# Performance work log

Measured on AMD Instinct MI355X. Metric: run time of the kernel, lower is better.

## Reference

```python
import jax, jax.numpy as jnp
import numpy as np

B, N, C, K = 16, 2048, 64, 20
RED = 16  # SE reduction


def setup_inputs() -> dict:
    key = jax.random.key(0)
    ks = jax.random.split(key, 8)
    x = jax.random.normal(ks[0], (B * N, C), dtype=jnp.float32)
    batch = jnp.repeat(jnp.arange(B, dtype=jnp.int64), N)
    s1 = 1.0 / np.sqrt(2 * C)
    s2 = 1.0 / np.sqrt(C)
    W1 = jax.random.normal(ks[1], (2 * C, C), dtype=jnp.float32) * s1
    b1 = jnp.zeros((C,), dtype=jnp.float32)
    W2 = jax.random.normal(ks[2], (C, C), dtype=jnp.float32) * s2
    b2 = jnp.zeros((C,), dtype=jnp.float32)
    W3 = jax.random.normal(ks[3], (C, C), dtype=jnp.float32) * s2
    b3 = jnp.zeros((C,), dtype=jnp.float32)
    se_w1 = jax.random.normal(ks[4], (C, C // RED), dtype=jnp.float32) * s2
    se_w2 = jax.random.normal(ks[5], (C // RED, C), dtype=jnp.float32) * (1.0 / np.sqrt(C // RED))
    sa_w = jax.random.normal(ks[6], (1, 2, 7), dtype=jnp.float32) * (1.0 / np.sqrt(14))
    return {"x": x, "batch": batch, "batch_size": B, "W1": W1, "b1": b1,
            "W2": W2, "b2": b2, "W3": W3, "b3": b3,
            "se_w1": se_w1, "se_w2": se_w2, "sa_w": sa_w}


def _forward(x, batch_size, W1, b1, W2, b2, W3, b3, se_w1, se_w2, sa_w):
    n = x.shape[0] // batch_size
    xb = x.reshape(batch_size, n, -1)              # [B,N,C]
    # --- dynamic kNN graph (self point included, as in PyG knn) ---
    sq = jnp.sum(xb * xb, axis=-1)                 # [B,N]
    d = sq[:, :, None] + sq[:, None, :] - 2.0 * jnp.einsum('bic,bjc->bij', xb, xb)
    _, idx = jax.lax.top_k(-d, K)                  # [B,N,K] nearest (incl self)
    xj = jax.vmap(lambda pts, ids: pts[ids])(xb, idx)   # [B,N,K,C]
    xi = xb[:, :, None, :]
    edge = jnp.concatenate([jnp.broadcast_to(xi, xj.shape), xj - xi], axis=-1)  # [B,N,K,2C]
    # --- shared edge MLP ---
    h = jax.nn.relu(edge @ W1 + b1)
    h = jax.nn.relu(h @ W2 + b2)
    h = h @ W3 + b3                                 # [B,N,K,C]
    agg = jnp.max(h, axis=2)                        # [B,N,C] max-aggregate
    # --- SE channel attention (pool over points) ---
    s = jnp.mean(agg, axis=1)                       # [B,C]
    y = jax.nn.sigmoid(jax.nn.relu(s @ se_w1) @ se_w2)  # [B,C]
    x_se = agg * y[:, None, :]
    # --- spatial attention (pool over channels, conv1d k=7) ---
    avg_out = jnp.mean(x_se, axis=2)                # [B,N]
    max_out = jnp.max(x_se, axis=2)                 # [B,N]
    ycat = jnp.stack([avg_out, max_out], axis=1)    # [B,2,N]
    att = jax.lax.conv_general_dilated(ycat, sa_w, (1,), [(3, 3)],
                                       dimension_numbers=('NCH', 'OIH', 'NCH'))  # [B,1,N]
    att = jax.nn.sigmoid(att)
    x_att = x_se * att.transpose(0, 2, 1)           # [B,N,C]
    # --- residual (in_channels == out_channels) ---
    out = x_att + xb
    return out.reshape(batch_size * n, -1)


def reference(x, batch, batch_size, W1, b1, W2, b2, W3, b3, se_w1, se_w2, sa_w):
    return _forward(x, batch_size, W1, b1, W2, b2, W3, b3, se_w1, se_w2, sa_w)
```

## Files before the change

### kernel.cpp

```cpp
#include <hip/hip_runtime.h>

typedef unsigned int uint32;
typedef unsigned long long uint64;
typedef unsigned short ushortT;
typedef __attribute__((ext_vector_type(8))) short short8;
typedef __attribute__((ext_vector_type(4))) short short4v;
typedef __attribute__((ext_vector_type(4))) float floatx4;

#define DEV static __device__ __forceinline__

#define NN 2048
#define CC 64
#define KK 20

DEV float bf2f(ushortT h) {
  union { uint32 u; float f; } c; c.u = ((uint32)h) << 16; return c.f;
}
DEV ushortT f2bf(float f) {
  union { float f; uint32 u; } c; c.f = f;
  uint32 r = c.u + 0x7FFFu + ((c.u >> 16) & 1u);
  return (ushortT)(r >> 16);
}
DEV void split2(float v, ushortT& h, ushortT& l) {
  h = f2bf(v);
  l = f2bf(v - bf2f(h));
}
DEV uint32 fmap(float f) {
  uint32 u = __float_as_uint(f);
  return (u & 0x80000000u) ? ~u : (u | 0x80000000u);
}
DEV float funmap(uint32 m) {
  uint32 u = (m & 0x80000000u) ? (m ^ 0x80000000u) : ~m;
  return __uint_as_float(u);
}
DEV short8 ld8(const ushortT* p) {
  short4v a = *(const short4v*)p;
  short4v b = *(const short4v*)(p + 4);
  short8 r;
  r[0] = a.x; r[1] = a.y; r[2] = a.z; r[3] = a.w;
  r[4] = b.x; r[5] = b.y; r[6] = b.z; r[7] = b.w;
  return r;
}

__global__ void k_sq(const float* __restrict__ x, float* __restrict__ sq,
                     ushortT* __restrict__ xbf) {
  int p = blockIdx.x * 256 + threadIdx.x;
  const float4* row = (const float4*)(x + (size_t)p * CC);
  ushortT* orow = xbf + (size_t)p * CC;
  float s = 0.f;
#pragma unroll
  for (int q = 0; q < 16; ++q) {
    float4 v = row[q];
    s += v.x * v.x + v.y * v.y + v.z * v.z + v.w * v.w;
    short4v h;
    h.x = (short)f2bf(v.x); h.y = (short)f2bf(v.y);
    h.z = (short)f2bf(v.z); h.w = (short)f2bf(v.w);
    *(short4v*)(orow + q * 4) = h;
  }
  sq[p] = s;
}

__global__ void k_wconv(const float* __restrict__ w1, const float* __restrict__ w2,
                        const float* __restrict__ w3, ushortT* __restrict__ wbf) {
  int t = threadIdx.x;
  for (int e = t; e < 4096; e += 256) {
    int n = e >> 6, k = e & 63;
    wbf[e]         = f2bf(w1[k * 64 + n]);
    wbf[4096 + e]  = f2bf(w1[(64 + k) * 64 + n]);
    wbf[8192 + e]  = f2bf(w2[k * 64 + n]);
    wbf[12288 + e] = f2bf(w3[k * 64 + n]);
  }
}

__launch_bounds__(256, 4)
__global__ void k_knn(const ushortT* __restrict__ xbf, const float* __restrict__ sq,
                      ushortT* __restrict__ cand) {
  const int b  = blockIdx.y;
  const int i0 = blockIdx.x * 32;
  const int t  = threadIdx.x;
  const int l  = t & 63, wv = t >> 6;
  const int la = l & 15, quad = l >> 4;
  const int pp = t >> 2, ss = t & 3;

  __shared__ __align__(16) char sm[35968];
  ushortT (*sXj)[72]    = (ushortT(*)[72])(sm);
  uint32  (*sCand)[130] = (uint32(*)[130])(sm + 18432);
  uint32*  sTau         = (uint32*)(sm + 35072);
  uint32*  sCnt         = (uint32*)(sm + 35200);
  float*   sSqi         = (float*)(sm + 35328);
  float*   sSqj         = (float*)(sm + 35456);

  const ushortT* xbb = xbf + ((size_t)b * NN) * CC;

  const int mw  = wv & 1;
  const int nt0 = (wv >> 1) * 4;

  short8 afrag[2];
  {
    const ushortT* rowp = xbb + (size_t)(i0 + mw * 16 + la) * CC;
#pragma unroll
    for (int ks = 0; ks < 2; ++ks)
      afrag[ks] = *(const short8*)(rowp + ks * 32 + quad * 8);
  }
  if (t < 32) sSqi[t] = sq[b * NN + i0 + t];

  {
    int r = t >> 1, co = (t & 1) * 32;
    const ushortT* src = xbb + (size_t)r * CC + co;
#pragma unroll
    for (int i = 0; i < 4; ++i)
      *(uint4*)&sXj[r][co + i * 8] = *(const uint4*)(src + i * 8);
  }
  if (t < 128) sSqj[t] = sq[b * NN + t];

  uint32 lst[KK];
#pragma unroll
  for (int s = 0; s < KK; ++s) lst[s] = 0xFFFFFFFFu;

  __syncthreads();

  float sqa[4];
  {
    float4 v = *(const float4*)&sSqi[mw * 16 + quad * 4];
    sqa[0] = v.x; sqa[1] = v.y; sqa[2] = v.z; sqa[3] = v.w;
  }

  for (int jt = 0; jt < 16; ++jt) {
    const int j0 = jt * 128;

    floatx4 acc[4];
#pragma unroll
    for (int n = 0; n < 4; ++n) acc[n] = (floatx4){0.f, 0.f, 0.f, 0.f};

#pragma unroll
    for (int ks = 0; ks < 2; ++ks) {
      int kof = ks * 32 + quad * 8;
#pragma unroll
      for (int n = 0; n < 4; ++n) {
        short8 bv = *(const short8*)&sXj[(nt0 + n) * 16 + la][kof];
        acc[n] = __builtin_amdgcn_mfma_f32_16x16x32_bf16(afrag[ks], bv, acc[n], 0, 0, 0);
      }
    }

    if (jt == 0) {
#pragma unroll
      for (int n = 0; n < 4; ++n) {
        int jl = (nt0 + n) * 16 + la;
        float dj = sSqj[jl];
        uint32 jg = (uint32)(j0 + jl);
#pragma unroll
        for (int rg = 0; rg < 4; ++rg) {
          int il = mw * 16 + quad * 4 + rg;
          float d = fmaxf(sqa[rg] + dj - 2.0f * acc[n][rg], 0.f);
          sCand[il][jl] = (__float_as_uint(d) & 0xFFFFF800u) | jg;
        }
      }
    } else {
      uint32 tv[4];
      {
        uint4 u = *(const uint4*)&sTau[mw * 16 + quad * 4];
        tv[0] = u.x; tv[1] = u.y; tv[2] = u.z; tv[3] = u.w;
      }
#pragma unroll
      for (int n = 0; n < 4; ++n) {
        int jl = (nt0 + n) * 16 + la;
        float dj = sSqj[jl];
        uint32 jg = (uint32)(j0 + jl);
#pragma unroll
        for (int rg = 0; rg < 4; ++rg) {
          int il = mw * 16 + quad * 4 + rg;
          float d = fmaxf(sqa[rg] + dj - 2.0f * acc[n][rg], 0.f);
          uint32 key = (__float_as_uint(d) & 0xFFFFF800u) | jg;
          if (key < tv[rg]) {
            uint32 slot = atomicAdd(&sCnt[il], 1u);
            sCand[il][slot] = key;
          }
        }
      }
    }
    __syncthreads();

    if (t < 128) {
      int cnt = (jt == 0) ? 128 : (int)sCnt[pp];
      for (int q = ss; q < cnt; q += 4) {
        uint32 cur = sCand[pp][q];
#pragma unroll
        for (int s = 0; s < KK; ++s) {
          uint32 lo = min(lst[s], cur);
          cur = max(lst[s], cur);
          lst[s] = lo;
        }
      }
      uint32 m19 = lst[KK - 1];
      m19 = min(m19, (uint32)__shfl_xor((int)m19, 1));
      m19 = min(m19, (uint32)__shfl_xor((int)m19, 2));
      if (ss == 0) { sTau[pp] = m19; sCnt[pp] = 0u; }
    }

    if (jt < 15) {
      const int jn = (jt + 1) * 128;
      int r = t >> 1, co = (t & 1) * 32;
      const ushortT* src = xbb + (size_t)(jn + r) * CC + co;
#pragma unroll
      for (int i = 0; i < 4; ++i)
        *(uint4*)&sXj[r][co + i * 8] = *(const uint4*)(src + i * 8);
      if (t < 128) sSqj[t] = sq[b * NN + jn + t];
    }
    __syncthreads();
  }

  if (t < 128) {
    size_t base = ((size_t)(b * NN + i0 + pp)) * 80 + ss * KK;
#pragma unroll
    for (int s = 0; s < KK; ++s) cand[base + s] = (ushortT)(lst[s] & 2047u);
  }
}

__launch_bounds__(256, 4)
__global__ void k_rerank(const float* __restrict__ x, const ushortT* __restrict__ cand,
                         int* __restrict__ idxout) {
  const int b  = blockIdx.y;
  const int i0 = blockIdx.x * 16;
  const int t  = threadIdx.x;
  const int grp = t >> 4, lg = t & 15;

  __shared__ double sK[16][81];

  const float* xb = x + ((size_t)b * NN) * CC;
  const int p = i0 + grp;
  float4 vi = ((const float4*)(xb + (size_t)p * CC))[lg];
  size_t cb = ((size_t)(b * NN + p)) * 80;

  const bool hi8 = (lg & 8) != 0;
  const bool hi4 = (lg & 4) != 0;
  const bool hi2 = (lg & 2) != 0;
  const int  uslot = ((lg >> 1) & 1) | (((lg >> 2) & 1) << 1) | (((lg >> 3) & 1) << 2);

  for (int q0 = 0; q0 < 80; q0 += 8) {
    int jj0 = (int)cand[cb + q0 + 0], jj1 = (int)cand[cb + q0 + 1];
    int jj2 = (int)cand[cb + q0 + 2], jj3 = (int)cand[cb + q0 + 3];
    int jj4 = (int)cand[cb + q0 + 4], jj5 = (int)cand[cb + q0 + 5];
    int jj6 = (int)cand[cb + q0 + 6], jj7 = (int)cand[cb + q0 + 7];

#define DISTQ(JJ, DD)                                                        \
    double DD;                                                               \
    {                                                                        \
      float4 vj = ((const float4*)(xb + (size_t)(JJ) * CC))[lg];             \
      double e0 = (double)vi.x - (double)vj.x;                               \
      double e1 = (double)vi.y - (double)vj.y;                               \
      double e2 = (double)vi.z - (double)vj.z;                               \
      double e3 = (double)vi.w - (double)vj.w;                               \
      DD = e0 * e0 + e1 * e1 + e2 * e2 + e3 * e3;                            \
    }
    DISTQ(jj0, dd0) DISTQ(jj1, dd1) DISTQ(jj2, dd2) DISTQ(jj3, dd3)
    DISTQ(jj4, dd4) DISTQ(jj5, dd5) DISTQ(jj6, dd6) DISTQ(jj7, dd7)
#undef DISTQ

    double m0 = hi8 ? dd4 : dd0, s0 = hi8 ? dd0 : dd4;
    double m1 = hi8 ? dd5 : dd1, s1 = hi8 ? dd1 : dd5;
    double m2 = hi8 ? dd6 : dd2, s2 = hi8 ? dd2 : dd6;
    double m3 = hi8 ? dd7 : dd3, s3 = hi8 ? dd3 : dd7;
    double r40 = m0 + __shfl_xor(s0, 8, 16);
    double r41 = m1 + __shfl_xor(s1, 8, 16);
    double r42 = m2 + __shfl_xor(s2, 8, 16);
    double r43 = m3 + __shfl_xor(s3, 8, 16);
    int j40 = hi8 ? jj4 : jj0, j41 = hi8 ? jj5 : jj1;
    int j42 = hi8 ? jj6 : jj2, j43 = hi8 ? jj7 : jj3;

    double n0 = hi4 ? r42 : r40, t0 = hi4 ? r40 : r42;
    double n1 = hi4 ? r43 : r41, t1 = hi4 ? r41 : r43;
    double r20 = n0 + __shfl_xor(t0, 4, 16);
    double r21 = n1 + __shfl_xor(t1, 4, 16);
    int j20 = hi4 ? j42 : j40, j21 = hi4 ? j43 : j41;

    double p0 = hi2 ? r21 : r20, u0 = hi2 ? r20 : r21;
    double r1 = p0 + __shfl_xor(u0, 2, 16);
    int j1 = hi2 ? j21 : j20;

    r1 += __shfl_xor(r1, 1, 16);

    if ((lg & 1) == 0) {
      uint64 bits = (uint64)__double_as_longlong(r1);
      sK[grp][q0 + uslot] = __longlong_as_double((bits & ~2047ULL) | (uint64)j1);
    }
  }
  __syncthreads();

  double k5[5];
#pragma unroll
  for (int s = 0; s < 5; ++s) k5[s] = sK[grp][lg + 16 * s];

  const double DINF = __longlong_as_double(0x7FF0000000000000LL);
  size_t obase = ((size_t)(b * NN + p)) * KK;
  for (int r = 0; r < KK; ++r) {
    double lm = fmin(fmin(fmin(k5[0], k5[1]), fmin(k5[2], k5[3])), k5[4]);
#pragma unroll
    for (int off = 8; off > 0; off >>= 1)
      lm = fmin(lm, __shfl_xor(lm, off, 16));
#pragma unroll
    for (int s = 0; s < 5; ++s) k5[s] = (k5[s] == lm) ? DINF : k5[s];
    if (lg == (r & 15))
      idxout[obase + r] = (int)((uint64)__double_as_longlong(lm) & 2047ULL);
  }
}

__launch_bounds__(256, 4)
__global__ void k_mlp(const float* __restrict__ x, const ushortT* __restrict__ xbf,
                      const int* __restrict__ idx, const ushortT* __restrict__ wbf,
                      const float* __restrict__ b1, const float* __restrict__ b2,
                      const float* __restrict__ b3, float* __restrict__ agg) {
  const int b  = blockIdx.y;
  const int i0 = blockIdx.x * 4;
  const int t  = threadIdx.x;
  const int l  = t & 63, wv = t >> 6;
  const int la = l & 15, quad = l >> 4;

  __shared__ __align__(16) char sm[35008];
  ushortT (*sDH)[68]  = (ushortT(*)[68])(sm + 0);
  ushortT (*sDL)[68]  = (ushortT(*)[68])(sm + 10880);
  ushortT (*sH1)[68]  = (ushortT(*)[68])(sm + 21760);
  float   (*sPre)[64] = (float(*)[64])(sm + 32640);
  uint32*  sAgg       = (uint32*)(sm + 33664);
  int*     sJ         = (int*)(sm + 34688);
  ushortT (*sH2)[68]  = sDH;

  const int c = wv * 16 + la;
  const ushortT* w1aT = wbf;
  const ushortT* w1bT = wbf + 4096;
  const ushortT* w2T  = wbf + 8192;
  const ushortT* w3T  = wbf + 12288;

  if (t < 80) {
    int p = t / 20, kk = t - p * 20;
    int v = idx[((size_t)(b * NN + i0 + p)) * KK + kk];
    v = v < 0 ? 0 : (v > (NN - 1) ? (NN - 1) : v);
    sJ[t] = v;
  }
  sAgg[t] = 0u;

  float b2c = b2[c], b3c = b3[c];

  {
    float b1c = b1[c];
    floatx4 ap = (floatx4){b1c, b1c, b1c, b1c};
#pragma unroll
    for (int ks = 0; ks < 2; ++ks) {
      short8 av = *(const short8*)(xbf + (size_t)(b * NN + i0 + (la & 3)) * CC + ks * 32 + quad * 8);
      short8 bv = *(const short8*)(w1aT + c * 64 + ks * 32 + quad * 8);
      ap = __builtin_amdgcn_mfma_f32_16x16x32_bf16(av, bv, ap, 0, 0, 0);
    }
    if (quad == 0) {
#pragma unroll
      for (int rg = 0; rg < 4; ++rg) sPre[rg][c] = ap[rg];
    }
  }
  __syncthreads();

  const float* xb = x + ((size_t)b * NN) * CC;
  for (int e = t; e < 1280; e += 256) {
    int r = e >> 4, c4g = e & 15, c4 = c4g * 4;
    int p = r / 20;
    float4 vi = ((const float4*)(xb + (size_t)(i0 + p) * CC))[c4g];
    float4 vj = ((const float4*)(xb + (size_t)sJ[r] * CC))[c4g];
    short4v dh, dl;
    ushortT hh, ll;
    split2(vj.x - vi.x, hh, ll); dh.x = (short)hh; dl.x = (short)ll;
    split2(vj.y - vi.y, hh, ll); dh.y = (short)hh; dl.y = (short)ll;
    split2(vj.z - vi.z, hh, ll); dh.z = (short)hh; dl.z = (short)ll;
    split2(vj.w - vi.w, hh, ll); dh.w = (short)hh; dl.w = (short)ll;
    *(short4v*)&sDH[r][c4] = dh;
    *(short4v*)&sDL[r][c4] = dl;
  }
  __syncthreads();

  {
    short8 bB[2];
#pragma unroll
    for (int ks = 0; ks < 2; ++ks)
      bB[ks] = *(const short8*)(w1bT + c * 64 + ks * 32 + quad * 8);
#pragma unroll
    for (int m5 = 0; m5 < 5; ++m5) {
      floatx4 a;
#pragma unroll
      for (int rg = 0; rg < 4; ++rg) {
        int r = m5 * 16 + quad * 4 + rg;
        a[rg] = sPre[r / 20][c];
      }
#pragma unroll
      for (int ks = 0; ks < 2; ++ks) {
        int kof = ks * 32 + quad * 8;
        short8 aDH = ld8(&sDH[m5 * 16 + la][kof]);
        short8 aDL = ld8(&sDL[m5 * 16 + la][kof]);
        a = __builtin_amdgcn_mfma_f32_16x16x32_bf16(aDH, bB[ks], a, 0, 0, 0);
        a = __builtin_amdgcn_mfma_f32_16x16x32_bf16(aDL, bB[ks], a, 0, 0, 0);
      }
#pragma unroll
      for (int rg = 0; rg < 4; ++rg) {
        int r = m5 * 16 + quad * 4 + rg;
        sH1[r][c] = f2bf(fmaxf(a[rg], 0.f));
      }
    }
  }
  __syncthreads();

  {
    short8 bf[2];
#pragma unroll
    for (int ks = 0; ks < 2; ++ks)
      bf[ks] = *(const short8*)(w2T + c * 64 + ks * 32 + quad * 8);
#pragma unroll
    for (int m5 = 0; m5 < 5; ++m5) {
      floatx4 a = (floatx4){b2c, b2c, b2c, b2c};
#pragma unroll
      for (int ks = 0; ks < 2; ++ks) {
        short8 aH = ld8(&sH1[m5 * 16 + la][ks * 32 + quad * 8]);
        a = __builtin_amdgcn_mfma_f32_16x16x32_bf16(aH, bf[ks], a, 0, 0, 0);
      }
#pragma unroll
      for (int rg = 0; rg < 4; ++rg) {
        int r = m5 * 16 + quad * 4 + rg;
        sH2[r][c] = f2bf(fmaxf(a[rg], 0.f));
      }
    }
  }
  __syncthreads();

  {
    short8 bf[2];
#pragma unroll
    for (int ks = 0; ks < 2; ++ks)
      bf[ks] = *(const short8*)(w3T + c * 64 + ks * 32 + quad * 8);
#pragma unroll
    for (int m5 = 0; m5 < 5; ++m5) {
      floatx4 a = (floatx4){b3c, b3c, b3c, b3c};
#pragma unroll
      for (int ks = 0; ks < 2; ++ks) {
        short8 aH = ld8(&sH2[m5 * 16 + la][ks * 32 + quad * 8]);
        a = __builtin_amdgcn_mfma_f32_16x16x32_bf16(aH, bf[ks], a, 0, 0, 0);
      }
#pragma unroll
      for (int rg = 0; rg < 4; ++rg) {
        int r = m5 * 16 + quad * 4 + rg;
        int p = r / 20;
        atomicMax(&sAgg[p * 64 + c], fmap(a[rg]));
      }
    }
  }
  __syncthreads();

  {
    int p = t >> 6, cc = t & 63;
    agg[((size_t)(b * NN + i0 + p)) * CC + cc] = funmap(sAgg[t]);
  }
}

__global__ void k_se1(const float* __restrict__ agg, float* __restrict__ part) {
  int b = blockIdx.x >> 4, ch = blockIdx.x & 15;
  int t = threadIdx.x;
  int c = t & 63, q = t >> 6;
  __shared__ float red[4][64];
  const float* ab = agg + ((size_t)(b * NN) + ch * 128) * CC;
  float s = 0.f;
  for (int r = q * 32; r < q * 32 + 32; ++r) s += ab[(size_t)r * CC + c];
  red[q][c] = s;
  __syncthreads();
  if (t < 64)
    part[blockIdx.x * 64 + t] = (red[0][t] + red[1][t]) + (red[2][t] + red[3][t]);
}

__global__ void k_se2(const float* __restrict__ part, const float* __restrict__ sew1,
                      const float* __restrict__ sew2, float* __restrict__ y) {
  int b = blockIdx.x, t = threadIdx.x;
  __shared__ float sv[64];
  __shared__ float hid[4];
  {
    float s = 0.f;
#pragma unroll
    for (int k = 0; k < 16; ++k) s += part[(b * 16 + k) * 64 + t];
    sv[t] = s * (1.f / 2048.f);
  }
  __syncthreads();
  if (t < 4) {
    float a = 0.f;
    for (int cc = 0; cc < 64; ++cc) a += sv[cc] * sew1[cc * 4 + t];
    hid[t] = fmaxf(a, 0.f);
  }
  __syncthreads();
  {
    float a = 0.f;
#pragma unroll
    for (int h = 0; h < 4; ++h) a += hid[h] * sew2[h * 64 + t];
    y[b * 64 + t] = 1.f / (1.f + expf(-a));
  }
}

__global__ void k_stats(const float* __restrict__ agg, const float* __restrict__ y,
                        float* __restrict__ ycat) {
  int t = threadIdx.x;
  int gid = blockIdx.x * 4 + (t >> 6);
  int l = t & 63;
  int b = gid >> 11, i = gid & 2047;
  float v = agg[(size_t)gid * CC + l] * y[b * 64 + l];
  float s = v, mx = v;
#pragma unroll
  for (int off = 32; off > 0; off >>= 1) {
    s += __shfl_xor(s, off);
    mx = fmaxf(mx, __shfl_xor(mx, off));
  }
  if (l == 0) {
    ycat[b * 2 * NN + i] = s * (1.f / 64.f);
    ycat[b * 2 * NN + NN + i] = mx;
  }
}

__global__ void k_final(const float* __restrict__ agg, const float* __restrict__ y,
                        const float* __restrict__ ycat, const float* __restrict__ saw,
                        const float* __restrict__ x, float* __restrict__ out) {
  int e = blockIdx.x * 256 + threadIdx.x;
  int ifl = e >> 6, c = e & 63;
  int b = ifl >> 11, i = ifl & 2047;
  float a = 0.f;
#pragma unroll
  for (int w = 0; w < 7; ++w) {
    int ii = i + w - 3;
    if (ii >= 0 && ii < NN) {
      a += ycat[b * 2 * NN + ii] * saw[w];
      a += ycat[b * 2 * NN + NN + ii] * saw[7 + w];
    }
  }
  float att = 1.f / (1.f + expf(-a));
  out[e] = agg[(size_t)ifl * CC + c] * y[b * 64 + c] * att + x[(size_t)e];
}

extern "C" void kernel_launch(void* const* d_in, const int* in_sizes, int n_in,
                              void* d_out, int out_size, void* d_ws, size_t ws_size,
                              hipStream_t stream) {
  const float* x    = (const float*)d_in[0];
  const float* w1   = (const float*)d_in[3];
  const float* b1   = (const float*)d_in[4];
  const float* w2   = (const float*)d_in[5];
  const float* b2   = (const float*)d_in[6];
  const float* w3   = (const float*)d_in[7];
  const float* b3   = (const float*)d_in[8];
  const float* sew1 = (const float*)d_in[9];
  const float* sew2 = (const float*)d_in[10];
  const float* saw  = (const float*)d_in[11];
  float* out = (float*)d_out;

  char* ws = (char*)d_ws;
  float*   sq   = (float*)  (ws);
  int*     idx  = (int*)    (ws + 131072);
  float*   part = (float*)  (ws + 131072);
  ushortT* cand = (ushortT*)(ws + 2752512);
  float*   agg  = (float*)  (ws + 2752512);
  float*   y    = (float*)  (ws + 11141120);
  float*   ycat = (float*)  (ws + 11145216);
  ushortT* wbf  = (ushortT*)(ws + 11407360);

  ushortT* xbf = (ushortT*)d_out;

  k_wconv <<<1,              256, 0, stream>>>(w1, w2, w3, wbf);
  k_sq    <<<128,            256, 0, stream>>>(x, sq, xbf);
  k_knn   <<<dim3(64, 16),   256, 0, stream>>>(xbf, sq, cand);
  k_rerank<<<dim3(128, 16),  256, 0, stream>>>(x, cand, idx);
  k_mlp   <<<dim3(512, 16),  256, 0, stream>>>(x, xbf, idx, wbf, b1, b2, b3, agg);
  k_se1   <<<256,            256, 0, stream>>>(agg, part);
  k_se2   <<<16,             64,  0, stream>>>(part, sew1, sew2, y);
  k_stats <<<8192,           256, 0, stream>>>(agg, y, ycat);
  k_final <<<8192,           256, 0, stream>>>(agg, y, ycat, saw, x, out);
}
```

Before: 305.5 us.

## Aggregate candidate atomics per wave, prefetch next tile, skip non-improving inserts

Per-lane LDS atomicAdd calls for candidate slots are replaced with one ballot-based atomic per 16-lane group. Each lane then writes its candidate at a rank computed by popcount. The global loads for the next j-tile are issued into registers before the top-K insertion phase and stored to LDS afterward, so their latency overlaps the selection work. The insertion network is skipped for candidates that cannot beat the current 20th-best. This adds register pressure for the four prefetched uint4 values and adds ballot/shuffle overhead.

Result: slower. 332.1 us (+8.7%).

```diff
diff --git a/kernel.cpp b/kernel.cpp
--- a/kernel.cpp
+++ b/kernel.cpp
@@ -125,6 +125,8 @@
     sqa[0] = v.x; sqa[1] = v.y; sqa[2] = v.z; sqa[3] = v.w;
   }
 
+  const int pr = t >> 1, pco = (t & 1) * 32;
+
   for (int jt = 0; jt < 16; ++jt) {
     const int j0 = jt * 128;
 
@@ -171,24 +173,47 @@
           int il = mw * 16 + quad * 4 + rg;
           float d = fmaxf(sqa[rg] + dj - 2.0f * acc[n][rg], 0.f);
           uint32 key = (__float_as_uint(d) & 0xFFFFF800u) | jg;
-          if (key < tv[rg]) {
-            uint32 slot = atomicAdd(&sCnt[il], 1u);
-            sCand[il][slot] = key;
+          bool ok = key < tv[rg];
+          uint64 wm = __ballot(ok);
+          uint32 gm = (uint32)((wm >> (quad * 16)) & 0xFFFFu);
+          if (gm) {
+            int leader = quad * 16 + (__ffs(gm) - 1);
+            uint32 base = 0;
+            if (l == leader) base = atomicAdd(&sCnt[il], (uint32)__popc(gm));
+            base = (uint32)__shfl((int)base, leader);
+            if (ok) {
+              uint32 rank = (uint32)__popc(gm & ((1u << la) - 1u));
+              sCand[il][base + rank] = key;
+            }
           }
         }
       }
     }
     __syncthreads();
+
+    uint4 pf0, pf1, pf2, pf3;
+    float sqpf = 0.f;
+    const bool havepf = (jt < 15);
+    if (havepf) {
+      const ushortT* src = xbb + (size_t)((jt + 1) * 128 + pr) * CC + pco;
+      pf0 = *(const uint4*)(src);
+      pf1 = *(const uint4*)(src + 8);
+      pf2 = *(const uint4*)(src + 16);
+      pf3 = *(const uint4*)(src + 24);
+      if (t < 128) sqpf = sq[b * NN + (jt + 1) * 128 + t];
+    }
 
     if (t < 128) {
       int cnt = (jt == 0) ? 128 : (int)sCnt[pp];
       for (int q = ss; q < cnt; q += 4) {
         uint32 cur = sCand[pp][q];
-#pragma unroll
-        for (int s = 0; s < KK; ++s) {
-          uint32 lo = min(lst[s], cur);
-          cur = max(lst[s], cur);
-          lst[s] = lo;
+        if (cur < lst[KK - 1]) {
+#pragma unroll
+          for (int s = 0; s < KK; ++s) {
+            uint32 lo = min(lst[s], cur);
+            cur = max(lst[s], cur);
+            lst[s] = lo;
+          }
         }
       }
       uint32 m19 = lst[KK - 1];
@@ -197,14 +222,12 @@
       if (ss == 0) { sTau[pp] = m19; sCnt[pp] = 0u; }
     }
 
-    if (jt < 15) {
-      const int jn = (jt + 1) * 128;
-      int r = t >> 1, co = (t & 1) * 32;
-      const ushortT* src = xbb + (size_t)(jn + r) * CC + co;
-#pragma unroll
-      for (int i = 0; i < 4; ++i)
-        *(uint4*)&sXj[r][co + i * 8] = *(const uint4*)(src + i * 8);
-      if (t < 128) sSqj[t] = sq[b * NN + jn + t];
+    if (havepf) {
+      *(uint4*)&sXj[pr][pco]      = pf0;
+      *(uint4*)&sXj[pr][pco + 8]  = pf1;
+      *(uint4*)&sXj[pr][pco + 16] = pf2;
+      *(uint4*)&sXj[pr][pco + 24] = pf3;
+      if (t < 128) sSqj[t] = sqpf;
     }
     __syncthreads();
   }
```
